# Performance work log

Measured on AMD Instinct MI355X. Metric: run time of the kernel, lower is better.

Reference implementation:

```python
import jax, jax.numpy as jnp
import numpy as np

N, M, K, D = 65536, 131072, 8, 64
TAU = 0.3
EPS = 1e-6

def setup_inputs() -> dict:
    key = jax.random.key(0)
    ks = jax.random.split(key, 16)
    s = 0.05
    return {
        "f_pts": jax.random.normal(ks[0], (N, D), jnp.float32),
        "pts": jax.random.uniform(ks[1], (N, 3), jnp.float32) * 10.0,
        "z_latent": jax.random.normal(ks[2], (M, D), jnp.float32) * 0.1,
        "centers": jax.random.uniform(ks[3], (M, 3), jnp.float32) * 10.0,
        "cand_idx": jax.random.randint(ks[4], (N, K), 0, M),
        "sim_w1": jax.random.normal(ks[5], (2 * D + 3, 64), jnp.float32) * s,
        "sim_b1": jnp.zeros((64,), jnp.float32),
        "sim_w2": jax.random.normal(ks[6], (64, 1), jnp.float32) * s,
        "sim_b2": jnp.zeros((1,), jnp.float32),
        "gate_w1": jax.random.normal(ks[7], (2 * D, D), jnp.float32) * s,
        "gate_b1": jnp.zeros((D,), jnp.float32),
        "gate_w2": jax.random.normal(ks[8], (D, 1), jnp.float32) * s,
        "gate_b2": jnp.zeros((1,), jnp.float32),
        "W_ih": jax.random.normal(ks[9], (3 * D, D), jnp.float32) * s,
        "W_hh": jax.random.normal(ks[10], (3 * D, D), jnp.float32) * s,
        "b_ih": jnp.zeros((3 * D,), jnp.float32),
        "b_hh": jnp.zeros((3 * D,), jnp.float32),
    }

def _forward(f_pts, pts, z_latent, centers, sim_w1, sim_b1, sim_w2, sim_b2,
             gate_w1, gate_b1, gate_w2, gate_b2, W_ih, W_hh, b_ih, b_hh, cand_idx):
    n, k = cand_idx.shape
    m, d = z_latent.shape
    # --- gather voxel latents / centers for each (point, candidate) pair ---
    z_c = z_latent[cand_idx]                         # (N,K,D)
    delta = pts[:, None, :] - centers[cand_idx]      # (N,K,3)
    f_b = jnp.broadcast_to(f_pts[:, None, :], (n, k, d))
    # --- similarity MLP ---
    x = jnp.concatenate([f_b, z_c, delta], axis=-1)  # (N,K,2D+3)
    h = jax.nn.relu(x @ sim_w1 + sim_b1)
    sim = (h @ sim_w2 + sim_b2)[..., 0]              # (N,K)
    # --- low-temperature top-K routing weights over candidates ---
    w = jax.nn.softmax(sim / TAU, axis=-1)           # (N,K)
    # --- scatter weighted point features to voxels ---
    flat_idx = cand_idx.reshape(-1)                  # (N*K,)
    contrib = (w[..., None] * f_pts[:, None, :]).reshape(-1, d)
    msg = jax.ops.segment_sum(contrib, flat_idx, num_segments=m)     # (M,D)
    wsum = jax.ops.segment_sum(w.reshape(-1), flat_idx, num_segments=m)
    msg = msg / (wsum[:, None] + EPS)                # normalized voxel message
    # --- per-voxel gate ---
    g_in = jnp.concatenate([z_latent, msg], axis=-1)
    gate = jax.nn.sigmoid(jax.nn.relu(g_in @ gate_w1 + gate_b1) @ gate_w2 + gate_b2)  # (M,1)
    # --- GRUCell (torch layout: rows ordered r,z,n) ---
    gi = msg @ W_ih.T + b_ih
    gh = z_latent @ W_hh.T + b_hh
    i_r, i_z, i_n = jnp.split(gi, 3, axis=-1)
    h_r, h_z, h_n = jnp.split(gh, 3, axis=-1)
    r = jax.nn.sigmoid(i_r + h_r)
    zg = jax.nn.sigmoid(i_z + h_z)
    nn_ = jnp.tanh(i_n + r * h_n)
    h_new = (1.0 - zg) * nn_ + zg * z_latent
    # gated latent update
    return z_latent + gate * (h_new - z_latent)

def reference(f_pts, pts, z_latent, centers, cand_idx, sim_w1, sim_b1, sim_w2, sim_b2,
              gate_w1, gate_b1, gate_w2, gate_b2, W_ih, W_hh, b_ih, b_hh):
    return _forward(f_pts, pts, z_latent, centers, sim_w1, sim_b1, sim_w2, sim_b2,
                    gate_w1, gate_b1, gate_w2, gate_b2, W_ih, W_hh, b_ih, b_hh, cand_idx)
```

## Files before the change

### kernel.cpp

```cpp
#include <hip/hip_runtime.h>
#include <hip/hip_fp16.h>
#include <math.h>


typedef short bf16x8 __attribute__((ext_vector_type(8)));
typedef unsigned short u16x8 __attribute__((ext_vector_type(8)));
typedef float f32x4 __attribute__((ext_vector_type(4)));
#define MFMA __builtin_amdgcn_mfma_f32_16x16x32_bf16
#define CAP 32

__device__ __forceinline__ short f2bf(float f) {
  unsigned u = __float_as_uint(f);
  unsigned r = (u + 0x7FFFu + ((u >> 16) & 1u)) >> 16;
  return (short)r;
}

__device__ __forceinline__ float bf2f(unsigned short h) {
  return __uint_as_float(((unsigned)h) << 16);
}

__device__ __forceinline__ float sigm(float x) { return 1.0f / (1.0f + __expf(-x)); }

__global__ __launch_bounds__(256) void prep_kernel(
    const float* __restrict__ z, const float* __restrict__ f,
    const float* __restrict__ sim_w1, const float* __restrict__ sim_b1,
    const float* __restrict__ gate_w1, const float* __restrict__ W_ih,
    const float* __restrict__ W_hh,
    unsigned short* __restrict__ zbf, unsigned short* __restrict__ fbf,
    unsigned short* __restrict__ HBt, short* __restrict__ bfZ,
    short* __restrict__ GF, short* __restrict__ WihF, short* __restrict__ WhhF,
    int* __restrict__ cursor, int M)
{
  long tid = (long)blockIdx.x * 256 + threadIdx.x;
  long nthr = (long)gridDim.x * 256;

  for (long i = tid; i < M; i += nthr) cursor[i] = 0;

  long nz = (long)M * 64;
  for (long i = tid * 8; i < nz; i += nthr * 8) {
    float4 a = *(const float4*)&z[i];
    float4 b4 = *(const float4*)&z[i + 4];
    u16x8 o;
    o[0] = (unsigned short)f2bf(a.x);  o[1] = (unsigned short)f2bf(a.y);
    o[2] = (unsigned short)f2bf(a.z);  o[3] = (unsigned short)f2bf(a.w);
    o[4] = (unsigned short)f2bf(b4.x); o[5] = (unsigned short)f2bf(b4.y);
    o[6] = (unsigned short)f2bf(b4.z); o[7] = (unsigned short)f2bf(b4.w);
    *(u16x8*)&zbf[i] = o;
  }

  if (blockIdx.x == gridDim.x - 1 && threadIdx.x < 64) {
    int lane = threadIdx.x;
    int lr = lane & 15, lg = lane >> 4;
#pragma unroll
    for (int ct = 0; ct < 4; ++ct)
#pragma unroll
      for (int kt = 0; kt < 3; ++kt) {
        bf16x8 b;
#pragma unroll
        for (int e = 0; e < 8; ++e) {
          int k = kt * 32 + lg * 8 + e;
          float v = (k < 67) ? sim_w1[(64 + k) * 64 + ct * 16 + lr] : 0.0f;
          b[e] = f2bf(v);
        }
        *(bf16x8*)&bfZ[(ct * 3 + kt) * 512 + lane * 8] = b;
      }
  }

  if (blockIdx.x >= 1024 && blockIdx.x < 1040) {
    int fb = (blockIdx.x - 1024) * 4 + (threadIdx.x >> 6);
    int lane = threadIdx.x & 63, lr = lane & 15, lg = lane >> 4;
    bf16x8 o;
    if (fb < 16) {
      int ct = fb >> 2, kt = fb & 3;
#pragma unroll
      for (int e = 0; e < 8; ++e)
        o[e] = f2bf(gate_w1[(kt * 32 + lg * 8 + e) * 64 + ct * 16 + lr]);
      *(bf16x8*)&GF[fb * 512 + lane * 8] = o;
    } else if (fb < 40) {
      int q = fb - 16, g = q >> 3, ct = (q >> 1) & 3, k2 = q & 1;
      int row = g * 64 + ct * 16 + lr;
#pragma unroll
      for (int e = 0; e < 8; ++e)
        o[e] = f2bf(W_ih[row * 64 + k2 * 32 + lg * 8 + e]);
      *(bf16x8*)&WihF[q * 512 + lane * 8] = o;
    } else {
      int q = fb - 40, g = q >> 3, ct = (q >> 1) & 3, k2 = q & 1;
      int row = g * 64 + ct * 16 + lr;
#pragma unroll
      for (int e = 0; e < 8; ++e)
        o[e] = f2bf(W_hh[row * 64 + k2 * 32 + lg * 8 + e]);
      *(bf16x8*)&WhhF[q * 512 + lane * 8] = o;
    }
  }

  {
    int g = blockIdx.x * 4 + (threadIdx.x >> 6);
    if ((g & 1) == 0) {
      int wave = g >> 1;
      int lane = threadIdx.x & 63;
      int lr = lane & 15, lg = lane >> 4;
      int n0 = wave * 16;

      bf16x8 bf[8];
#pragma unroll
      for (int ct = 0; ct < 4; ++ct)
#pragma unroll
        for (int kt = 0; kt < 2; ++kt) {
          bf16x8 bb;
#pragma unroll
          for (int e = 0; e < 8; ++e)
            bb[e] = f2bf(sim_w1[(kt * 32 + lg * 8 + e) * 64 + ct * 16 + lr]);
          bf[ct * 2 + kt] = bb;
        }

      bf16x8 a[2];
#pragma unroll
      for (int kt = 0; kt < 2; ++kt) {
        const float* src = &f[(long)(n0 + lr) * 64 + kt * 32 + lg * 8];
        float4 v0 = *(const float4*)src;
        float4 v1 = *(const float4*)(src + 4);
        bf16x8 t;
        t[0] = f2bf(v0.x); t[1] = f2bf(v0.y); t[2] = f2bf(v0.z); t[3] = f2bf(v0.w);
        t[4] = f2bf(v1.x); t[5] = f2bf(v1.y); t[6] = f2bf(v1.z); t[7] = f2bf(v1.w);
        a[kt] = t;
      }
      *(bf16x8*)&fbf[(long)(n0 + lr) * 64 + lg * 8] = a[0];
      *(bf16x8*)&fbf[(long)(n0 + lr) * 64 + 32 + lg * 8] = a[1];

      f32x4 acc[4] = {{0,0,0,0},{0,0,0,0},{0,0,0,0},{0,0,0,0}};
#pragma unroll
      for (int ct = 0; ct < 4; ++ct) {
        acc[ct] = MFMA(a[0], bf[ct * 2 + 0], acc[ct], 0, 0, 0);
        acc[ct] = MFMA(a[1], bf[ct * 2 + 1], acc[ct], 0, 0, 0);
      }
      float b10 = sim_b1[lr], b11 = sim_b1[16 + lr];
      float b12 = sim_b1[32 + lr], b13 = sim_b1[48 + lr];
#pragma unroll
      for (int e = 0; e < 4; ++e) {
        unsigned lo = (unsigned)(unsigned short)f2bf(acc[0][e] + b10)
                    | ((unsigned)(unsigned short)f2bf(acc[1][e] + b11) << 16);
        unsigned hi = (unsigned)(unsigned short)f2bf(acc[2][e] + b12)
                    | ((unsigned)(unsigned short)f2bf(acc[3][e] + b13) << 16);
        *(uint2*)&HBt[(long)(n0 + lg * 4 + e) * 64 + lr * 4] = make_uint2(lo, hi);
      }
    }
  }
}

#define TPW 4
__global__ __launch_bounds__(256) void pair_kernel(
    const float* __restrict__ pts, const unsigned short* __restrict__ zbf,
    const float* __restrict__ centers, const int* __restrict__ cand_idx,
    const float* __restrict__ sim_w2, const short* __restrict__ bfZ,
    const unsigned short* __restrict__ HBt,
    int* __restrict__ cursor, unsigned* __restrict__ rec)
{
  int wave = (blockIdx.x * 256 + threadIdx.x) >> 6;
  int lane = threadIdx.x & 63;
  int lr = lane & 15, lg = lane >> 4;

  int call = cand_idx[wave * 64 + lane];

  bf16x8 b[12];
#pragma unroll
  for (int i = 0; i < 12; ++i) b[i] = *(const bf16x8*)&bfZ[i * 512 + lane * 8];
  float w2c[4];
#pragma unroll
  for (int ct = 0; ct < 4; ++ct) w2c[ct] = sim_w2[ct * 16 + lr];

  int c[TPW];
  bf16x8 a0[TPW], a1[TPW], ad[TPW];
  uint2 h2[TPW];
#pragma unroll
  for (int t = 0; t < TPW; ++t) {
    c[t] = __shfl(call, t * 16 + lr, 64);
    a0[t] = *(const bf16x8*)&zbf[(long)c[t] * 64 + lg * 8];
    a1[t] = *(const bf16x8*)&zbf[(long)c[t] * 64 + 32 + lg * 8];
    h2[t] = *(const uint2*)&HBt[((long)(wave * TPW + t) * 2 + (lg >> 1)) * 64 + lr * 4];
    bf16x8 tt = {0, 0, 0, 0, 0, 0, 0, 0};
    if (lg == 0) {
      int n = (wave * TPW + t) * 2 + (lr >> 3);
      tt[0] = f2bf(pts[n * 3 + 0] - centers[c[t] * 3 + 0]);
      tt[1] = f2bf(pts[n * 3 + 1] - centers[c[t] * 3 + 1]);
      tt[2] = f2bf(pts[n * 3 + 2] - centers[c[t] * 3 + 2]);
    }
    ad[t] = tt;
  }

  f32x4 part[TPW];
#pragma unroll
  for (int t = 0; t < TPW; ++t) {
    f32x4 acc[4] = {{0,0,0,0},{0,0,0,0},{0,0,0,0},{0,0,0,0}};
#pragma unroll
    for (int ct = 0; ct < 4; ++ct) {
      acc[ct] = MFMA(a0[t], b[ct * 3 + 0], acc[ct], 0, 0, 0);
      acc[ct] = MFMA(a1[t], b[ct * 3 + 1], acc[ct], 0, 0, 0);
      acc[ct] = MFMA(ad[t], b[ct * 3 + 2], acc[ct], 0, 0, 0);
    }
    float hb[4];
    hb[0] = bf2f((unsigned short)(h2[t].x));
    hb[1] = bf2f((unsigned short)(h2[t].x >> 16));
    hb[2] = bf2f((unsigned short)(h2[t].y));
    hb[3] = bf2f((unsigned short)(h2[t].y >> 16));
    f32x4 p = {0.f, 0.f, 0.f, 0.f};
#pragma unroll
    for (int ct = 0; ct < 4; ++ct)
#pragma unroll
      for (int e = 0; e < 4; ++e)
        p[e] = fmaf(fmaxf(acc[ct][e] + hb[ct], 0.0f), w2c[ct], p[e]);
    part[t] = p;
  }

  float wrow[TPW];
#pragma unroll
  for (int t = 0; t < TPW; ++t) {
    f32x4 p = part[t];
#pragma unroll
    for (int m = 1; m <= 8; m <<= 1)
#pragma unroll
      for (int e = 0; e < 4; ++e) p[e] += __shfl_xor(p[e], m, 64);
    float other[4];
#pragma unroll
    for (int e = 0; e < 4; ++e) other[e] = __shfl_xor(p[e], 16, 64);
    float mx = p[0];
#pragma unroll
    for (int e = 1; e < 4; ++e) mx = fmaxf(mx, p[e]);
#pragma unroll
    for (int e = 0; e < 4; ++e) mx = fmaxf(mx, other[e]);
    float ex[4], se = 0.f, so = 0.f;
#pragma unroll
    for (int e = 0; e < 4; ++e) {
      ex[e] = __expf((p[e] - mx) * (1.0f / 0.3f));
      se += ex[e];
      so += __expf((other[e] - mx) * (1.0f / 0.3f));
    }
    float inv = 1.0f / (se + so);
    int srcl = (lane >> 2) << 4;
    float t0 = __shfl(ex[0] * inv, srcl, 64);
    float t1 = __shfl(ex[1] * inv, srcl, 64);
    float t2 = __shfl(ex[2] * inv, srcl, 64);
    float t3 = __shfl(ex[3] * inv, srcl, 64);
    int esel = lane & 3;
    wrow[t] = esel == 0 ? t0 : esel == 1 ? t1 : esel == 2 ? t2 : t3;
  }

  int slot = atomicAdd(&cursor[call], 1);

  float v0 = __shfl(wrow[0], lr, 64);
  float v1 = __shfl(wrow[1], lr, 64);
  float v2 = __shfl(wrow[2], lr, 64);
  float v3 = __shfl(wrow[3], lr, 64);
  float wv = lg == 0 ? v0 : lg == 1 ? v1 : lg == 2 ? v2 : v3;

  if (slot < CAP) {
    int n_pt = wave * 8 + 2 * lg + (lr >> 3);
    unsigned short wh = __half_as_ushort(__float2half(wv));
    rec[(long)call * CAP + slot] = ((unsigned)n_pt << 16) | (unsigned)wh;
  }
}

__global__ __launch_bounds__(256) void gather_kernel(
    const unsigned* __restrict__ rec, const int* __restrict__ cursor,
    const unsigned short* __restrict__ fbf, unsigned short* __restrict__ msg_bf,
    int mvox)
{
  int tid = blockIdx.x * 256 + threadIdx.x;
  int row = tid >> 2, seg = tid & 3;
  if (row >= mvox) return;

  int cnt = cursor[row];
  cnt = cnt < CAP ? cnt : CAP;
  const unsigned* rp = &rec[(long)row * CAP];

  float acc[16];
#pragma unroll
  for (int j = 0; j < 16; ++j) acc[j] = 0.f;
  float ws = 0.f;

  for (int i0 = 0; i0 < cnt; i0 += 4) {
    uint4 r4 = *(const uint4*)&rp[i0];
    unsigned rr0 = r4.x, rr1 = r4.y, rr2 = r4.z, rr3 = r4.w;
#pragma unroll
    for (int j = 0; j < 4; ++j) {
      unsigned r = j == 0 ? rr0 : j == 1 ? rr1 : j == 2 ? rr2 : rr3;
      if (i0 + j < cnt) {
        float w = __half2float(__ushort_as_half((unsigned short)(r & 0xffffu)));
        int n = r >> 16;
        ws += w;
        const u16x8* fp = (const u16x8*)&fbf[(long)n * 64 + seg * 16];
        u16x8 f0 = fp[0], f1 = fp[1];
#pragma unroll
        for (int k = 0; k < 8; ++k) {
          acc[k]     = fmaf(w, bf2f(f0[k]), acc[k]);
          acc[8 + k] = fmaf(w, bf2f(f1[k]), acc[8 + k]);
        }
      }
    }
  }
  float inv = 1.0f / (ws + 1e-6f);
  u16x8 o0, o1;
#pragma unroll
  for (int j = 0; j < 8; ++j) {
    o0[j] = (unsigned short)f2bf(acc[j] * inv);
    o1[j] = (unsigned short)f2bf(acc[8 + j] * inv);
  }
  *(u16x8*)&msg_bf[(long)row * 64 + seg * 16] = o0;
  *(u16x8*)&msg_bf[(long)row * 64 + seg * 16 + 8] = o1;
}

__global__ __launch_bounds__(512)
__attribute__((amdgpu_waves_per_eu(2)))
void stage2(
    const unsigned short* __restrict__ zbf,
    const short* __restrict__ GF, const short* __restrict__ WihF,
    const short* __restrict__ WhhF,
    const float* __restrict__ gate_b1, const float* __restrict__ gate_w2,
    const float* __restrict__ gate_b2,
    const float* __restrict__ b_ih, const float* __restrict__ b_hh,
    const unsigned short* __restrict__ msg_bf,
    float* __restrict__ out)
{
  __shared__ float gb1s[64], gw2s[64], bihs[192], bhhs[192];
  __shared__ float gb2s;

  int t = threadIdx.x;
  if (t < 64) { gb1s[t] = gate_b1[t]; gw2s[t] = gate_w2[t]; }
  if (t < 192) { bihs[t] = b_ih[t]; bhhs[t] = b_hh[t]; }
  if (t == 0) gb2s = gate_b2[0];
  __syncthreads();

  int wid = t >> 6, lane = t & 63;
  int lr = lane & 15, lg = lane >> 4;

  int rowbase = blockIdx.x * 128 + wid * 16;
  long abase = (long)(rowbase + lr) * 64;
  bf16x8 a0 = *(const bf16x8*)&zbf[abase + lg * 8];
  bf16x8 a1 = *(const bf16x8*)&zbf[abase + 32 + lg * 8];
  bf16x8 a2 = *(const bf16x8*)&msg_bf[abase + lg * 8];
  bf16x8 a3 = *(const bf16x8*)&msg_bf[abase + 32 + lg * 8];

  f32x4 usum = {0.f, 0.f, 0.f, 0.f};
#pragma unroll 1
  for (int ct = 0; ct < 4; ++ct) {
    f32x4 au = {0, 0, 0, 0};
    au = MFMA(a0, *(const bf16x8*)&GF[(ct * 4 + 0) * 512 + lane * 8], au, 0, 0, 0);
    au = MFMA(a1, *(const bf16x8*)&GF[(ct * 4 + 1) * 512 + lane * 8], au, 0, 0, 0);
    au = MFMA(a2, *(const bf16x8*)&GF[(ct * 4 + 2) * 512 + lane * 8], au, 0, 0, 0);
    au = MFMA(a3, *(const bf16x8*)&GF[(ct * 4 + 3) * 512 + lane * 8], au, 0, 0, 0);
    int c = ct * 16 + lr;
#pragma unroll
    for (int e = 0; e < 4; ++e)
      usum[e] += fmaxf(au[e] + gb1s[c], 0.0f) * gw2s[c];
  }
#pragma unroll
  for (int m = 1; m <= 8; m <<= 1)
#pragma unroll
    for (int e = 0; e < 4; ++e) {
      float v = usum[e];
      usum[e] = v + __shfl_xor(v, m, 64);
    }
  float gate[4];
#pragma unroll
  for (int e = 0; e < 4; ++e) gate[e] = sigm(usum[e] + gb2s);

#pragma unroll 1
  for (int ct = 0; ct < 4; ++ct) {
    f32x4 air = {0,0,0,0}, aiz = {0,0,0,0}, ain = {0,0,0,0};
    f32x4 ahr = {0,0,0,0}, ahz = {0,0,0,0}, ahn = {0,0,0,0};
#pragma unroll
    for (int k2 = 0; k2 < 2; ++k2) {
      bf16x8 amg = k2 ? a3 : a2;
      bf16x8 az_ = k2 ? a1 : a0;
      int base = ct * 2 + k2;
      air = MFMA(amg, *(const bf16x8*)&WihF[(      base) * 512 + lane * 8], air, 0, 0, 0);
      aiz = MFMA(amg, *(const bf16x8*)&WihF[( 8 +  base) * 512 + lane * 8], aiz, 0, 0, 0);
      ain = MFMA(amg, *(const bf16x8*)&WihF[(16 +  base) * 512 + lane * 8], ain, 0, 0, 0);
      ahr = MFMA(az_, *(const bf16x8*)&WhhF[(      base) * 512 + lane * 8], ahr, 0, 0, 0);
      ahz = MFMA(az_, *(const bf16x8*)&WhhF[( 8 +  base) * 512 + lane * 8], ahz, 0, 0, 0);
      ahn = MFMA(az_, *(const bf16x8*)&WhhF[(16 +  base) * 512 + lane * 8], ahn, 0, 0, 0);
    }
    int c = ct * 16 + lr;
#pragma unroll
    for (int e = 0; e < 4; ++e) {
      float zv = bf2f(zbf[(long)(rowbase + lg * 4 + e) * 64 + c]);
      float rr = sigm(air[e] + bihs[c] + ahr[e] + bhhs[c]);
      float zg = sigm(aiz[e] + bihs[64 + c] + ahz[e] + bhhs[64 + c]);
      float nn = tanhf(ain[e] + bihs[128 + c] + rr * (ahn[e] + bhhs[128 + c]));
      float hnew = (1.0f - zg) * nn + zg * zv;
      out[(long)(rowbase + lg * 4 + e) * 64 + c] = zv + gate[e] * (hnew - zv);
    }
  }
}

extern "C" void kernel_launch(void* const* d_in, const int* in_sizes, int n_in,
                              void* d_out, int out_size, void* d_ws, size_t ws_size,
                              hipStream_t stream) {
  const float* f_pts   = (const float*)d_in[0];
  const float* pts     = (const float*)d_in[1];
  const float* z_lat   = (const float*)d_in[2];
  const float* centers = (const float*)d_in[3];
  const int*   cand    = (const int*)d_in[4];
  const float* sim_w1  = (const float*)d_in[5];
  const float* sim_b1  = (const float*)d_in[6];
  const float* sim_w2  = (const float*)d_in[7];
  const float* gate_w1 = (const float*)d_in[9];
  const float* gate_b1 = (const float*)d_in[10];
  const float* gate_w2 = (const float*)d_in[11];
  const float* gate_b2 = (const float*)d_in[12];
  const float* W_ih    = (const float*)d_in[13];
  const float* W_hh    = (const float*)d_in[14];
  const float* b_ih    = (const float*)d_in[15];
  const float* b_hh    = (const float*)d_in[16];

  int N = in_sizes[0] / 64;
  int M = in_sizes[2] / 64;

  int* cursor = (int*)d_ws;
  unsigned* rec = (unsigned*)(cursor + M);
  unsigned short* msg_bf = (unsigned short*)rec;
  unsigned short* zbf = (unsigned short*)(rec + (size_t)M * CAP);
  unsigned short* fbf = zbf + (size_t)M * 64;
  unsigned short* HBt = fbf + (size_t)N * 64;
  short* bfZ = (short*)(HBt + (size_t)N * 64);
  short* GF = bfZ + 12 * 512;
  short* WihF = GF + 16 * 512;
  short* WhhF = WihF + 24 * 512;

  prep_kernel<<<2048, 256, 0, stream>>>(z_lat, f_pts, sim_w1, sim_b1,
                                        gate_w1, W_ih, W_hh,
                                        zbf, fbf, HBt, bfZ, GF, WihF, WhhF,
                                        cursor, M);

  int nwaves = (N * 8) / (16 * TPW);
  pair_kernel<<<nwaves / 4, 256, 0, stream>>>(pts, zbf, centers, cand,
                                              sim_w2, bfZ, HBt, cursor, rec);

  gather_kernel<<<(M * 4) / 256, 256, 0, stream>>>(rec, cursor, fbf, msg_bf, M);

  stage2<<<M / 128, 512, 0, stream>>>(zbf, GF, WihF, WhhF,
                                      gate_b1, gate_w2, gate_b2, b_ih, b_hh,
                                      msg_bf, (float*)d_out);
}
```

Before: 108.6 us.

## Precompute per-voxel first-layer projection so pair stage only gathers and adds

The similarity MLP's first layer is split linearly: per-point f·W_f + pts·W_d + b and per-voxel z·W_z − centers·W_d are each computed once in the prep kernel, not once per (point, candidate) pair. The pair kernel now gathers a 64-wide bf16 row per candidate, adds it to the point row, and applies relu, the dot with w2 and the softmax with one wave per point. This removes the per-pair MFMA work and replaces the 128-byte zbf gathers with ZC row gathers, but adds an M×64 projection pass and an extra rounding of the pts−centers term. Each point's delta is rounded to bf16 as two separate large terms instead of one small difference, which may lose precision.

```diff
diff --git a/kernel.cpp b/kernel.cpp
--- a/kernel.cpp
+++ b/kernel.cpp
@@ -23,11 +23,12 @@
 
 __global__ __launch_bounds__(256) void prep_kernel(
     const float* __restrict__ z, const float* __restrict__ f,
+    const float* __restrict__ pts, const float* __restrict__ centers,
     const float* __restrict__ sim_w1, const float* __restrict__ sim_b1,
     const float* __restrict__ gate_w1, const float* __restrict__ W_ih,
     const float* __restrict__ W_hh,
     unsigned short* __restrict__ zbf, unsigned short* __restrict__ fbf,
-    unsigned short* __restrict__ HBt, short* __restrict__ bfZ,
+    unsigned short* __restrict__ HBp, unsigned short* __restrict__ ZC,
     short* __restrict__ GF, short* __restrict__ WihF, short* __restrict__ WhhF,
     int* __restrict__ cursor, int M)
 {
@@ -48,24 +49,6 @@
     *(u16x8*)&zbf[i] = o;
   }
 
-  if (blockIdx.x == gridDim.x - 1 && threadIdx.x < 64) {
-    int lane = threadIdx.x;
-    int lr = lane & 15, lg = lane >> 4;
-#pragma unroll
-    for (int ct = 0; ct < 4; ++ct)
-#pragma unroll
-      for (int kt = 0; kt < 3; ++kt) {
-        bf16x8 b;
-#pragma unroll
-        for (int e = 0; e < 8; ++e) {
-          int k = kt * 32 + lg * 8 + e;
-          float v = (k < 67) ? sim_w1[(64 + k) * 64 + ct * 16 + lr] : 0.0f;
-          b[e] = f2bf(v);
-        }
-        *(bf16x8*)&bfZ[(ct * 3 + kt) * 512 + lane * 8] = b;
-      }
-  }
-
   if (blockIdx.x >= 1024 && blockIdx.x < 1040) {
     int fb = (blockIdx.x - 1024) * 4 + (threadIdx.x >> 6);
     int lane = threadIdx.x & 63, lr = lane & 15, lg = lane >> 4;
@@ -93,169 +76,192 @@
     }
   }
 
-  {
-    int g = blockIdx.x * 4 + (threadIdx.x >> 6);
-    if ((g & 1) == 0) {
-      int wave = g >> 1;
-      int lane = threadIdx.x & 63;
-      int lr = lane & 15, lg = lane >> 4;
-      int n0 = wave * 16;
-
-      bf16x8 bf[8];
-#pragma unroll
-      for (int ct = 0; ct < 4; ++ct)
-#pragma unroll
-        for (int kt = 0; kt < 2; ++kt) {
-          bf16x8 bb;
-#pragma unroll
-          for (int e = 0; e < 8; ++e)
-            bb[e] = f2bf(sim_w1[(kt * 32 + lg * 8 + e) * 64 + ct * 16 + lr]);
-          bf[ct * 2 + kt] = bb;
-        }
-
-      bf16x8 a[2];
+  int g = blockIdx.x * 4 + (threadIdx.x >> 6);
+  int lane = threadIdx.x & 63;
+  int lr = lane & 15, lg = lane >> 4;
+
+  if (g < 4096) {
+    int n0 = g * 16;
+    bf16x8 bw[12];
+#pragma unroll
+    for (int ct = 0; ct < 4; ++ct) {
 #pragma unroll
       for (int kt = 0; kt < 2; ++kt) {
-        const float* src = &f[(long)(n0 + lr) * 64 + kt * 32 + lg * 8];
-        float4 v0 = *(const float4*)src;
-        float4 v1 = *(const float4*)(src + 4);
-        bf16x8 t;
-        t[0] = f2bf(v0.x); t[1] = f2bf(v0.y); t[2] = f2bf(v0.z); t[3] = f2bf(v0.w);
-        t[4] = f2bf(v1.x); t[5] = f2bf(v1.y); t[6] = f2bf(v1.z); t[7] = f2bf(v1.w);
-        a[kt] = t;
-      }
-      *(bf16x8*)&fbf[(long)(n0 + lr) * 64 + lg * 8] = a[0];
-      *(bf16x8*)&fbf[(long)(n0 + lr) * 64 + 32 + lg * 8] = a[1];
-
-      f32x4 acc[4] = {{0,0,0,0},{0,0,0,0},{0,0,0,0},{0,0,0,0}};
-#pragma unroll
-      for (int ct = 0; ct < 4; ++ct) {
-        acc[ct] = MFMA(a[0], bf[ct * 2 + 0], acc[ct], 0, 0, 0);
-        acc[ct] = MFMA(a[1], bf[ct * 2 + 1], acc[ct], 0, 0, 0);
-      }
-      float b10 = sim_b1[lr], b11 = sim_b1[16 + lr];
-      float b12 = sim_b1[32 + lr], b13 = sim_b1[48 + lr];
-#pragma unroll
-      for (int e = 0; e < 4; ++e) {
-        unsigned lo = (unsigned)(unsigned short)f2bf(acc[0][e] + b10)
-                    | ((unsigned)(unsigned short)f2bf(acc[1][e] + b11) << 16);
-        unsigned hi = (unsigned)(unsigned short)f2bf(acc[2][e] + b12)
-                    | ((unsigned)(unsigned short)f2bf(acc[3][e] + b13) << 16);
-        *(uint2*)&HBt[(long)(n0 + lg * 4 + e) * 64 + lr * 4] = make_uint2(lo, hi);
-      }
-    }
-  }
-}
-
-#define TPW 4
+        bf16x8 bb;
+#pragma unroll
+        for (int e = 0; e < 8; ++e)
+          bb[e] = f2bf(sim_w1[(kt * 32 + lg * 8 + e) * 64 + ct * 16 + lr]);
+        bw[ct * 3 + kt] = bb;
+      }
+      bf16x8 bb = {0,0,0,0,0,0,0,0};
+#pragma unroll
+      for (int e = 0; e < 8; ++e) {
+        int kk = lg * 8 + e;
+        if (kk < 3) bb[e] = f2bf(sim_w1[(128 + kk) * 64 + ct * 16 + lr]);
+      }
+      bw[ct * 3 + 2] = bb;
+    }
+
+    bf16x8 a[3];
+#pragma unroll
+    for (int kt = 0; kt < 2; ++kt) {
+      const float* src = &f[(long)(n0 + lr) * 64 + kt * 32 + lg * 8];
+      float4 v0 = *(const float4*)src;
+      float4 v1 = *(const float4*)(src + 4);
+      bf16x8 t;
+      t[0] = f2bf(v0.x); t[1] = f2bf(v0.y); t[2] = f2bf(v0.z); t[3] = f2bf(v0.w);
+      t[4] = f2bf(v1.x); t[5] = f2bf(v1.y); t[6] = f2bf(v1.z); t[7] = f2bf(v1.w);
+      a[kt] = t;
+    }
+    {
+      bf16x8 t = {0,0,0,0,0,0,0,0};
+      if (lg == 0) {
+        t[0] = f2bf(pts[(n0 + lr) * 3 + 0]);
+        t[1] = f2bf(pts[(n0 + lr) * 3 + 1]);
+        t[2] = f2bf(pts[(n0 + lr) * 3 + 2]);
+      }
+      a[2] = t;
+    }
+    *(bf16x8*)&fbf[(long)(n0 + lr) * 64 + lg * 8] = a[0];
+    *(bf16x8*)&fbf[(long)(n0 + lr) * 64 + 32 + lg * 8] = a[1];
+
+    f32x4 acc[4] = {{0,0,0,0},{0,0,0,0},{0,0,0,0},{0,0,0,0}};
+#pragma unroll
+    for (int ct = 0; ct < 4; ++ct)
+#pragma unroll
+      for (int kt = 0; kt < 3; ++kt)
+        acc[ct] = MFMA(a[kt], bw[ct * 3 + kt], acc[ct], 0, 0, 0);
+
+#pragma unroll
+    for (int ct = 0; ct < 4; ++ct) {
+      float b1 = sim_b1[ct * 16 + lr];
+#pragma unroll
+      for (int e = 0; e < 4; ++e)
+        HBp[(long)(n0 + lg * 4 + e) * 64 + ct * 16 + lr] =
+            (unsigned short)f2bf(acc[ct][e] + b1);
+    }
+  } else if (g < 12288) {
+    int r0 = (g - 4096) * 16;
+    bf16x8 bw[12];
+#pragma unroll
+    for (int ct = 0; ct < 4; ++ct) {
+#pragma unroll
+      for (int kt = 0; kt < 2; ++kt) {
+        bf16x8 bb;
+#pragma unroll
+        for (int e = 0; e < 8; ++e)
+          bb[e] = f2bf(sim_w1[(64 + kt * 32 + lg * 8 + e) * 64 + ct * 16 + lr]);
+        bw[ct * 3 + kt] = bb;
+      }
+      bf16x8 bb = {0,0,0,0,0,0,0,0};
+#pragma unroll
+      for (int e = 0; e < 8; ++e) {
+        int kk = lg * 8 + e;
+        if (kk < 3) bb[e] = f2bf(sim_w1[(128 + kk) * 64 + ct * 16 + lr]);
+      }
+      bw[ct * 3 + 2] = bb;
+    }
+
+    bf16x8 a[3];
+#pragma unroll
+    for (int kt = 0; kt < 2; ++kt) {
+      const float* src = &z[(long)(r0 + lr) * 64 + kt * 32 + lg * 8];
+      float4 v0 = *(const float4*)src;
+      float4 v1 = *(const float4*)(src + 4);
+      bf16x8 t;
+      t[0] = f2bf(v0.x); t[1] = f2bf(v0.y); t[2] = f2bf(v0.z); t[3] = f2bf(v0.w);
+      t[4] = f2bf(v1.x); t[5] = f2bf(v1.y); t[6] = f2bf(v1.z); t[7] = f2bf(v1.w);
+      a[kt] = t;
+    }
+    {
+      bf16x8 t = {0,0,0,0,0,0,0,0};
+      if (lg == 0) {
+        t[0] = f2bf(-centers[(r0 + lr) * 3 + 0]);
+        t[1] = f2bf(-centers[(r0 + lr) * 3 + 1]);
+        t[2] = f2bf(-centers[(r0 + lr) * 3 + 2]);
+      }
+      a[2] = t;
+    }
+
+    f32x4 acc[4] = {{0,0,0,0},{0,0,0,0},{0,0,0,0},{0,0,0,0}};
+#pragma unroll
+    for (int ct = 0; ct < 4; ++ct)
+#pragma unroll
+      for (int kt = 0; kt < 3; ++kt)
+        acc[ct] = MFMA(a[kt], bw[ct * 3 + kt], acc[ct], 0, 0, 0);
+
+#pragma unroll
+    for (int ct = 0; ct < 4; ++ct)
+#pragma unroll
+      for (int e = 0; e < 4; ++e)
+        ZC[(long)(r0 + lg * 4 + e) * 64 + ct * 16 + lr] =
+            (unsigned short)f2bf(acc[ct][e]);
+  }
+}
+
 __global__ __launch_bounds__(256) void pair_kernel(
-    const float* __restrict__ pts, const unsigned short* __restrict__ zbf,
-    const float* __restrict__ centers, const int* __restrict__ cand_idx,
-    const float* __restrict__ sim_w2, const short* __restrict__ bfZ,
-    const unsigned short* __restrict__ HBt,
+    const unsigned short* __restrict__ HBp, const unsigned short* __restrict__ ZC,
+    const int* __restrict__ cand_idx, const float* __restrict__ sim_w2,
     int* __restrict__ cursor, unsigned* __restrict__ rec)
 {
-  int wave = (blockIdx.x * 256 + threadIdx.x) >> 6;
+  int n = (blockIdx.x * 256 + threadIdx.x) >> 6;
   int lane = threadIdx.x & 63;
-  int lr = lane & 15, lg = lane >> 4;
-
-  int call = cand_idx[wave * 64 + lane];
-
-  bf16x8 b[12];
-#pragma unroll
-  for (int i = 0; i < 12; ++i) b[i] = *(const bf16x8*)&bfZ[i * 512 + lane * 8];
-  float w2c[4];
-#pragma unroll
-  for (int ct = 0; ct < 4; ++ct) w2c[ct] = sim_w2[ct * 16 + lr];
-
-  int c[TPW];
-  bf16x8 a0[TPW], a1[TPW], ad[TPW];
-  uint2 h2[TPW];
-#pragma unroll
-  for (int t = 0; t < TPW; ++t) {
-    c[t] = __shfl(call, t * 16 + lr, 64);
-    a0[t] = *(const bf16x8*)&zbf[(long)c[t] * 64 + lg * 8];
-    a1[t] = *(const bf16x8*)&zbf[(long)c[t] * 64 + 32 + lg * 8];
-    h2[t] = *(const uint2*)&HBt[((long)(wave * TPW + t) * 2 + (lg >> 1)) * 64 + lr * 4];
-    bf16x8 tt = {0, 0, 0, 0, 0, 0, 0, 0};
-    if (lg == 0) {
-      int n = (wave * TPW + t) * 2 + (lr >> 3);
-      tt[0] = f2bf(pts[n * 3 + 0] - centers[c[t] * 3 + 0]);
-      tt[1] = f2bf(pts[n * 3 + 1] - centers[c[t] * 3 + 1]);
-      tt[2] = f2bf(pts[n * 3 + 2] - centers[c[t] * 3 + 2]);
-    }
-    ad[t] = tt;
-  }
-
-  f32x4 part[TPW];
-#pragma unroll
-  for (int t = 0; t < TPW; ++t) {
-    f32x4 acc[4] = {{0,0,0,0},{0,0,0,0},{0,0,0,0},{0,0,0,0}};
-#pragma unroll
-    for (int ct = 0; ct < 4; ++ct) {
-      acc[ct] = MFMA(a0[t], b[ct * 3 + 0], acc[ct], 0, 0, 0);
-      acc[ct] = MFMA(a1[t], b[ct * 3 + 1], acc[ct], 0, 0, 0);
-      acc[ct] = MFMA(ad[t], b[ct * 3 + 2], acc[ct], 0, 0, 0);
-    }
-    float hb[4];
-    hb[0] = bf2f((unsigned short)(h2[t].x));
-    hb[1] = bf2f((unsigned short)(h2[t].x >> 16));
-    hb[2] = bf2f((unsigned short)(h2[t].y));
-    hb[3] = bf2f((unsigned short)(h2[t].y >> 16));
-    f32x4 p = {0.f, 0.f, 0.f, 0.f};
-#pragma unroll
-    for (int ct = 0; ct < 4; ++ct)
-#pragma unroll
-      for (int e = 0; e < 4; ++e)
-        p[e] = fmaf(fmaxf(acc[ct][e] + hb[ct], 0.0f), w2c[ct], p[e]);
-    part[t] = p;
-  }
-
-  float wrow[TPW];
-#pragma unroll
-  for (int t = 0; t < TPW; ++t) {
-    f32x4 p = part[t];
-#pragma unroll
-    for (int m = 1; m <= 8; m <<= 1)
-#pragma unroll
-      for (int e = 0; e < 4; ++e) p[e] += __shfl_xor(p[e], m, 64);
-    float other[4];
-#pragma unroll
-    for (int e = 0; e < 4; ++e) other[e] = __shfl_xor(p[e], 16, 64);
-    float mx = p[0];
-#pragma unroll
-    for (int e = 1; e < 4; ++e) mx = fmaxf(mx, p[e]);
-#pragma unroll
-    for (int e = 0; e < 4; ++e) mx = fmaxf(mx, other[e]);
-    float ex[4], se = 0.f, so = 0.f;
-#pragma unroll
-    for (int e = 0; e < 4; ++e) {
-      ex[e] = __expf((p[e] - mx) * (1.0f / 0.3f));
-      se += ex[e];
-      so += __expf((other[e] - mx) * (1.0f / 0.3f));
-    }
-    float inv = 1.0f / (se + so);
-    int srcl = (lane >> 2) << 4;
-    float t0 = __shfl(ex[0] * inv, srcl, 64);
-    float t1 = __shfl(ex[1] * inv, srcl, 64);
-    float t2 = __shfl(ex[2] * inv, srcl, 64);
-    float t3 = __shfl(ex[3] * inv, srcl, 64);
-    int esel = lane & 3;
-    wrow[t] = esel == 0 ? t0 : esel == 1 ? t1 : esel == 2 ? t2 : t3;
-  }
-
-  int slot = atomicAdd(&cursor[call], 1);
-
-  float v0 = __shfl(wrow[0], lr, 64);
-  float v1 = __shfl(wrow[1], lr, 64);
-  float v2 = __shfl(wrow[2], lr, 64);
-  float v3 = __shfl(wrow[3], lr, 64);
-  float wv = lg == 0 ? v0 : lg == 1 ? v1 : lg == 2 ? v2 : v3;
-
-  if (slot < CAP) {
-    int n_pt = wave * 8 + 2 * lg + (lr >> 3);
-    unsigned short wh = __half_as_ushort(__float2half(wv));
-    rec[(long)call * CAP + slot] = ((unsigned)n_pt << 16) | (unsigned)wh;
+
+  int ci = cand_idx[n * 8 + (lane & 7)];
+  int c0 = __builtin_amdgcn_readlane(ci, 0);
+  int c1 = __builtin_amdgcn_readlane(ci, 1);
+  int c2 = __builtin_amdgcn_readlane(ci, 2);
+  int c3 = __builtin_amdgcn_readlane(ci, 3);
+  int c4 = __builtin_amdgcn_readlane(ci, 4);
+  int c5 = __builtin_amdgcn_readlane(ci, 5);
+  int c6 = __builtin_amdgcn_readlane(ci, 6);
+  int c7 = __builtin_amdgcn_readlane(ci, 7);
+
+  float hbv = bf2f(HBp[(long)n * 64 + lane]);
+  float w2 = sim_w2[lane];
+  float p0 = fmaxf(hbv + bf2f(ZC[(long)c0 * 64 + lane]), 0.f) * w2;
+  float p1 = fmaxf(hbv + bf2f(ZC[(long)c1 * 64 + lane]), 0.f) * w2;
+  float p2 = fmaxf(hbv + bf2f(ZC[(long)c2 * 64 + lane]), 0.f) * w2;
+  float p3 = fmaxf(hbv + bf2f(ZC[(long)c3 * 64 + lane]), 0.f) * w2;
+  float p4 = fmaxf(hbv + bf2f(ZC[(long)c4 * 64 + lane]), 0.f) * w2;
+  float p5 = fmaxf(hbv + bf2f(ZC[(long)c5 * 64 + lane]), 0.f) * w2;
+  float p6 = fmaxf(hbv + bf2f(ZC[(long)c6 * 64 + lane]), 0.f) * w2;
+  float p7 = fmaxf(hbv + bf2f(ZC[(long)c7 * 64 + lane]), 0.f) * w2;
+
+#pragma unroll
+  for (int m = 1; m <= 32; m <<= 1) {
+    p0 += __shfl_xor(p0, m, 64);
+    p1 += __shfl_xor(p1, m, 64);
+    p2 += __shfl_xor(p2, m, 64);
+    p3 += __shfl_xor(p3, m, 64);
+    p4 += __shfl_xor(p4, m, 64);
+    p5 += __shfl_xor(p5, m, 64);
+    p6 += __shfl_xor(p6, m, 64);
+    p7 += __shfl_xor(p7, m, 64);
+  }
+
+  float mx = fmaxf(fmaxf(fmaxf(p0, p1), fmaxf(p2, p3)),
+                   fmaxf(fmaxf(p4, p5), fmaxf(p6, p7)));
+  float e0 = __expf((p0 - mx) * (1.0f / 0.3f));
+  float e1 = __expf((p1 - mx) * (1.0f / 0.3f));
+  float e2 = __expf((p2 - mx) * (1.0f / 0.3f));
+  float e3 = __expf((p3 - mx) * (1.0f / 0.3f));
+  float e4 = __expf((p4 - mx) * (1.0f / 0.3f));
+  float e5 = __expf((p5 - mx) * (1.0f / 0.3f));
+  float e6 = __expf((p6 - mx) * (1.0f / 0.3f));
+  float e7 = __expf((p7 - mx) * (1.0f / 0.3f));
+  float inv = 1.0f / (e0 + e1 + e2 + e3 + e4 + e5 + e6 + e7);
+
+  if (lane < 8) {
+    float wsel = lane == 0 ? e0 : lane == 1 ? e1 : lane == 2 ? e2 :
+                 lane == 3 ? e3 : lane == 4 ? e4 : lane == 5 ? e5 :
+                 lane == 6 ? e6 : e7;
+    wsel *= inv;
+    int slot = atomicAdd(&cursor[ci], 1);
+    if (slot < CAP) {
+      unsigned short wh = __half_as_ushort(__float2half(wsel));
+      rec[(long)ci * CAP + slot] = ((unsigned)n << 16) | (unsigned)wh;
+    }
   }
 }
 
@@ -285,9 +291,9 @@
       unsigned r = j == 0 ? rr0 : j == 1 ? rr1 : j == 2 ? rr2 : rr3;
       if (i0 + j < cnt) {
         float w = __half2float(__ushort_as_half((unsigned short)(r & 0xffffu)));
-        int n = r >> 16;
+        int nn = r >> 16;
         ws += w;
-        const u16x8* fp = (const u16x8*)&fbf[(long)n * 64 + seg * 16];
+        const u16x8* fp = (const u16x8*)&fbf[(long)nn * 64 + seg * 16];
         u16x8 f0 = fp[0], f1 = fp[1];
 #pragma unroll
         for (int k = 0; k < 8; ++k) {
@@ -420,20 +426,18 @@
   unsigned short* msg_bf = (unsigned short*)rec;
   unsigned short* zbf = (unsigned short*)(rec + (size_t)M * CAP);
   unsigned short* fbf = zbf + (size_t)M * 64;
-  unsigned short* HBt = fbf + (size_t)N * 64;
-  short* bfZ = (short*)(HBt + (size_t)N * 64);
-  short* GF = bfZ + 12 * 512;
+  unsigned short* HBp = fbf + (size_t)N * 64;
+  unsigned short* ZC = HBp + (size_t)N * 64;
+  short* GF = (short*)(ZC + (size_t)M * 64);
   short* WihF = GF + 16 * 512;
   short* WhhF = WihF + 24 * 512;
 
-  prep_kernel<<<2048, 256, 0, stream>>>(z_lat, f_pts, sim_w1, sim_b1,
-                                        gate_w1, W_ih, W_hh,
-                                        zbf, fbf, HBt, bfZ, GF, WihF, WhhF,
+  prep_kernel<<<3072, 256, 0, stream>>>(z_lat, f_pts, pts, centers,
+                                        sim_w1, sim_b1, gate_w1, W_ih, W_hh,
+                                        zbf, fbf, HBp, ZC, GF, WihF, WhhF,
                                         cursor, M);
 
-  int nwaves = (N * 8) / (16 * TPW);
-  pair_kernel<<<nwaves / 4, 256, 0, stream>>>(pts, zbf, centers, cand,
-                                              sim_w2, bfZ, HBt, cursor, rec);
+  pair_kernel<<<N / 4, 256, 0, stream>>>(HBp, ZC, cand, sim_w2, cursor, rec);
 
   gather_kernel<<<(M * 4) / 256, 256, 0, stream>>>(rec, cursor, fbf, msg_bf, M);
 
```

Result: slower. 119.3 us (+9.9%).
